# Performance work log

Measured on AMD Instinct MI355X. Metric: run time of the kernel, lower is better.

## Reference

```python
import jax, jax.numpy as jnp
import numpy as np

REG_M = 0.1     # reg_m_bregman
N_ITER = 30     # fixed MM iteration count (POT uses numItermax=1000 w/ early stop)
EPS = 1e-16     # POT's stabilizer added to the denominator


def setup_inputs() -> dict:
    key = jax.random.key(0)
    kx, ky = jax.random.split(key)
    x = jax.random.normal(kx, (4096, 256), dtype=jnp.float32)
    y = jax.random.normal(ky, (4096, 256), dtype=jnp.float32)
    # L2-normalize embeddings so squared distances lie in [0,4] and the
    # KL kernel exp(-M / (2*reg_m)) stays in a representable range.
    x = x / jnp.linalg.norm(x, axis=1, keepdims=True)
    y = y / jnp.linalg.norm(y, axis=1, keepdims=True)
    return {"x": x, "y": y}


def reference(x, y):
    m, n = x.shape[0], y.shape[0]
    # ot.dist default metric: squared euclidean  M[i,j] = ||x_i - y_j||^2
    M = (jnp.sum(x * x, axis=1)[:, None]
         + jnp.sum(y * y, axis=1)[None, :]
         - 2.0 * (x @ y.T))                                  # [m, n]
    a = jnp.full((m,), 1.0 / m, dtype=x.dtype)
    b = jnp.full((n,), 1.0 / n, dtype=x.dtype)
    # POT mm_unbalanced, div='kl', reg_m1=reg_m2=reg_m, reg=0:
    # r1 = r2 = 1/2, K = sqrt(a_i b_j) * exp(-M / (2*reg_m)), G0 = a (x) b,
    # G <- K * G / (sqrt(rowsum_i) * sqrt(colsum_j) + eps)
    K = jnp.sqrt(a[:, None] * b[None, :]) * jnp.exp(-M / (2.0 * REG_M))
    G0 = a[:, None] * b[None, :]

    def step(G, _):
        Gd = jnp.sqrt(G.sum(axis=1)[:, None] * G.sum(axis=0)[None, :]) + EPS
        return K * G / Gd, None

    Pi, _ = jax.lax.scan(step, G0, None, length=N_ITER)
    # (Pi @ M.T).mean() = sum_j (sum_i Pi[i,j]) * (sum_k M[k,j]) / m^2
    return jnp.dot(Pi.sum(axis=0), M.sum(axis=0)) / (m * m)
```

## Files before the change

### kernel.cpp

```cpp
#include <hip/hip_runtime.h>
#include <math.h>

#define MDIM 4096
#define NDIM 4096
#define DDIM 256
#define N_ITER 30

#define TWO_KAPPA 14.426950408889634
#define CLCONST  (-12.0 - TWO_KAPPA)

typedef __attribute__((ext_vector_type(8))) short bf16x8;
typedef __attribute__((ext_vector_type(4))) float f32x4;

__device__ __forceinline__ unsigned encf(float f) {
  unsigned u = __float_as_uint(f);
  return (u & 0x80000000u) ? ~u : (u | 0x80000000u);
}
__device__ __forceinline__ float decf(unsigned u) {
  return __uint_as_float((u & 0x80000000u) ? (u ^ 0x80000000u) : ~u);
}
__device__ __forceinline__ unsigned ldvu(const unsigned* p) { return *(const volatile unsigned*)p; }
__device__ __forceinline__ float    ldvf(const float* p)    { return *(const volatile float*)p; }

__global__ void norms_kernel(const float* __restrict__ x, const float* __restrict__ y,
                             float* __restrict__ xx, float* __restrict__ yy,
                             float* __restrict__ Sxx) {
  int wid = threadIdx.x >> 6, lane = threadIdx.x & 63;
  int row = blockIdx.x * 4 + wid;
  const float* src = (row < MDIM) ? x : y;
  int r = (row < MDIM) ? row : row - MDIM;
  const float4* p = (const float4*)(src + (size_t)r * DDIM);
  float4 v = p[lane];
  float s = v.x*v.x + v.y*v.y + v.z*v.z + v.w*v.w;
  #pragma unroll
  for (int off = 32; off; off >>= 1) s += __shfl_down(s, off);
  if (lane == 0) {
    if (row < MDIM) { xx[r] = s; atomicAdd(Sxx, s); }
    else            { yy[r] = s; }
  }
}

__global__ void sx_kernel(const float* __restrict__ x, float* __restrict__ sx) {
  int tx = threadIdx.x;
  int r0 = blockIdx.x * 16;
  float s = 0.f;
  #pragma unroll
  for (int r = 0; r < 16; ++r) s += x[(size_t)(r0 + r) * DDIM + tx];
  atomicAdd(&sx[tx], s);
}

__global__ void colM_kernel(const float* __restrict__ y, const float* __restrict__ sx,
                            const float* __restrict__ yy, const float* __restrict__ Sxx,
                            float* __restrict__ colM) {
  int wid = threadIdx.x >> 6, lane = threadIdx.x & 63;
  int j = blockIdx.x * 4 + wid;
  const float4* py = (const float4*)(y + (size_t)j * DDIM);
  const float4* ps = (const float4*)sx;
  float4 a = py[lane], b = ps[lane];
  float s = a.x*b.x + a.y*b.y + a.z*b.z + a.w*b.w;
  #pragma unroll
  for (int off = 32; off; off >>= 1) s += __shfl_down(s, off);
  if (lane == 0) colM[j] = *Sxx + (float)MDIM * yy[j] - 2.f * s;
}

__global__ void split_kernel(const float* __restrict__ x, const float* __restrict__ y,
                             ushort* __restrict__ xh, ushort* __restrict__ xl,
                             ushort* __restrict__ yh, ushort* __restrict__ yl) {
  int g = blockIdx.x * 256 + threadIdx.x;
  int e; const float4* src; ushort* dh; ushort* dl;
  if (g < 262144) { e = g;          src = (const float4*)x; dh = xh; dl = xl; }
  else            { e = g - 262144; src = (const float4*)y; dh = yh; dl = yl; }
  float4 v = src[e];
  float f[4] = {v.x, v.y, v.z, v.w};
  ushort hs[4], ls[4];
  #pragma unroll
  for (int i = 0; i < 4; ++i) {
    unsigned u = __float_as_uint(f[i]);
    unsigned hr = (u + 0x7FFFu + ((u >> 16) & 1u)) >> 16;
    hs[i] = (ushort)hr;
    float hf = __uint_as_float(hr << 16);
    float lo = f[i] - hf;
    unsigned ul = __float_as_uint(lo);
    unsigned lr = (ul + 0x7FFFu + ((ul >> 16) & 1u)) >> 16;
    ls[i] = (ushort)lr;
  }
  *(ushort4*)(dh + (size_t)e * 4) = make_ushort4(hs[0], hs[1], hs[2], hs[3]);
  *(ushort4*)(dl + (size_t)e * 4) = make_ushort4(ls[0], ls[1], ls[2], ls[3]);
}

#define GPAD 56
__global__ __launch_bounds__(256)
void gemm_mfma_kernel(const ushort* __restrict__ xh, const ushort* __restrict__ xl,
                      const ushort* __restrict__ yh, const ushort* __restrict__ yl,
                      short* __restrict__ D16, float* __restrict__ maxdot) {
  __shared__ ushort As[2][128][GPAD];
  __shared__ ushort Bs[2][128][GPAD];
  int tid = threadIdx.x;
  int lane = tid & 63, wid = tid >> 6;
  int bm = blockIdx.x & 31, bn = blockIdx.x >> 5;
  int wrow = (wid >> 1) * 64, wcol = (wid & 1) * 64;
  f32x4 acc[4][4] = {};

  int c0 = tid, c1 = tid + 256;
  int r0 = c0 >> 2, k80 = (c0 & 3) * 8;
  int r1 = c1 >> 2, k81 = (c1 & 3) * 8;
  const size_t arow0 = (size_t)(bm * 128 + r0) * DDIM;
  const size_t arow1 = (size_t)(bm * 128 + r1) * DDIM;
  const size_t brow0 = (size_t)(bn * 128 + r0) * DDIM;
  const size_t brow1 = (size_t)(bn * 128 + r1) * DDIM;

  for (int k0 = 0; k0 < DDIM; k0 += 32) {
    *(uint4*)&As[0][r0][k80] = *(const uint4*)(xh + arow0 + k0 + k80);
    *(uint4*)&As[0][r1][k81] = *(const uint4*)(xh + arow1 + k0 + k81);
    *(uint4*)&As[1][r0][k80] = *(const uint4*)(xl + arow0 + k0 + k80);
    *(uint4*)&As[1][r1][k81] = *(const uint4*)(xl + arow1 + k0 + k81);
    *(uint4*)&Bs[0][r0][k80] = *(const uint4*)(yh + brow0 + k0 + k80);
    *(uint4*)&Bs[0][r1][k81] = *(const uint4*)(yh + brow1 + k0 + k81);
    *(uint4*)&Bs[1][r0][k80] = *(const uint4*)(yl + brow0 + k0 + k80);
    *(uint4*)&Bs[1][r1][k81] = *(const uint4*)(yl + brow1 + k0 + k81);
    __syncthreads();
    int fr = lane & 15, kg = lane >> 4;
    bf16x8 ah[4], al[4], bh[4], bl[4];
    #pragma unroll
    for (int i = 0; i < 4; ++i) {
      ah[i] = *(const bf16x8*)&As[0][wrow + i * 16 + fr][kg * 8];
      al[i] = *(const bf16x8*)&As[1][wrow + i * 16 + fr][kg * 8];
      bh[i] = *(const bf16x8*)&Bs[0][wcol + i * 16 + fr][kg * 8];
      bl[i] = *(const bf16x8*)&Bs[1][wcol + i * 16 + fr][kg * 8];
    }
    #pragma unroll
    for (int i = 0; i < 4; ++i)
      #pragma unroll
      for (int j = 0; j < 4; ++j) {
        acc[i][j] = __builtin_amdgcn_mfma_f32_16x16x32_bf16(ah[i], bh[j], acc[i][j], 0, 0, 0);
        acc[i][j] = __builtin_amdgcn_mfma_f32_16x16x32_bf16(ah[i], bl[j], acc[i][j], 0, 0, 0);
        acc[i][j] = __builtin_amdgcn_mfma_f32_16x16x32_bf16(al[i], bh[j], acc[i][j], 0, 0, 0);
      }
    __syncthreads();
  }
  float tmax = -1.f;
  #pragma unroll
  for (int i = 0; i < 4; ++i) {
    #pragma unroll
    for (int j = 0; j < 4; ++j) {
      int col = bn * 128 + wcol + j * 16 + (lane & 15);
      #pragma unroll
      for (int r = 0; r < 4; ++r) {
        float d = acc[i][j][r];
        tmax = fmaxf(tmax, d);
        int q = __float2int_rn(fminf(fmaxf(d * 65536.f, -32767.f), 32767.f));
        int row = bm * 128 + wrow + i * 16 + (lane >> 4) * 4 + r;
        D16[(size_t)row * NDIM + col] = (short)q;
      }
    }
  }
  __shared__ float sm[4];
  #pragma unroll
  for (int off = 32; off; off >>= 1) tmax = fmaxf(tmax, __shfl_down(tmax, off));
  if (lane == 0) sm[wid] = tmax;
  __syncthreads();
  if (tid == 0) {
    float m = fmaxf(fmaxf(sm[0], sm[1]), fmaxf(sm[2], sm[3]));
    atomicMax((int*)maxdot, __float_as_int(fmaxf(m, 0.f)));
  }
}

__device__ __forceinline__ void gridbar(unsigned* cnt, unsigned* root, int b, int blk) {
  __syncthreads();
  if (threadIdx.x == 0) {
    unsigned* sc = cnt + ((b << 4) + (blk & 15)) * 16;
    unsigned old = __hip_atomic_fetch_add(sc, 1u, __ATOMIC_ACQ_REL, __HIP_MEMORY_SCOPE_AGENT);
    if (old == 15u) {
      __hip_atomic_fetch_add(root + b * 16, 1u, __ATOMIC_ACQ_REL, __HIP_MEMORY_SCOPE_AGENT);
    }
    while (__hip_atomic_load(root + b * 16, __ATOMIC_RELAXED, __HIP_MEMORY_SCOPE_AGENT) < 16u)
      __builtin_amdgcn_s_sleep(1);
    (void)__hip_atomic_load(root + b * 16, __ATOMIC_ACQUIRE, __HIP_MEMORY_SCOPE_AGENT);
  }
  __syncthreads();
}

__global__ __launch_bounds__(1024, 4)
void solve_kernel(const short* __restrict__ D16,
                  float* __restrict__ phi_g, float* __restrict__ psi_g,
                  const float* __restrict__ maxdot,
                  unsigned* psimaxS, unsigned* phimaxS,
                  const float* __restrict__ colM,
                  float* lossacc, float* __restrict__ out,
                  unsigned* cnt, unsigned* root) {
  __shared__ float vec_lds[4096];
  __shared__ float red[32][33];
  __shared__ float own[32];
  int tid = threadIdx.x;
  int blk = blockIdx.x;
  bool rowside = blk < 128;
  int lloc = tid & 31;
  int chunk = tid >> 5;
  int obase = (rowside ? blk : (blk - 128)) * 32;
  float md = maxdot[0];

  int2 d[32];
  if (rowside) {
    const short* src = D16 + (size_t)(obase + lloc) * NDIM + chunk * 128;
    #pragma unroll
    for (int g = 0; g < 32; ++g) d[g] = *(const int2*)(src + 4 * g);
  } else {
    int j = obase + lloc;
    #pragma unroll
    for (int g = 0; g < 32; ++g) {
      int rr = chunk * 128 + 4 * g;
      unsigned s0 = (unsigned short)(unsigned)D16[(size_t)(rr + 0) * NDIM + j];
      unsigned s1 = (unsigned short)(unsigned)D16[(size_t)(rr + 1) * NDIM + j];
      unsigned s2 = (unsigned short)(unsigned)D16[(size_t)(rr + 2) * NDIM + j];
      unsigned s3 = (unsigned short)(unsigned)D16[(size_t)(rr + 3) * NDIM + j];
      d[g].x = (int)(s0 | (s1 << 16));
      d[g].y = (int)(s2 | (s3 << 16));
    }
  }
  if (tid < 32) own[tid] = -6.f;

  for (int t = 1; t <= N_ITER; ++t) {
    float sD  = (float)((double)t * (TWO_KAPPA / 65536.0));
    float tCL = (float)((double)t * CLCONST);
    float s2k = (float)((double)t * TWO_KAPPA);
    float tLmax = fmaf(s2k, md, tCL);
    float psimax, phimax;
    if (t == 1) { psimax = phimax = -6.f; }
    else {
      unsigned up = 0, uf = 0;
      #pragma unroll
      for (int s = 0; s < 16; ++s) {
        unsigned a = ldvu(&psimaxS[(t << 4) + s]); up = a > up ? a : up;
        unsigned b = ldvu(&phimaxS[(t << 4) + s]); uf = b > uf ? b : uf;
      }
      psimax = decf(up); phimax = decf(uf);
    }
    float Sr = tLmax + psimax - 100.f;
    float Sc = tLmax + phimax - 100.f;
    float Wr = tCL - Sr;
    float Wc = tCL - Sc;
    float Sh = rowside ? Sr : Sc;

    {
      float add = rowside ? Wr : Wc;
      float4 v;
      if (t == 1) {
        float c = -6.f + add;
        v = make_float4(c, c, c, c);
      } else {
        const float* src = rowside ? psi_g : phi_g;
        v = *(const float4*)(src + tid * 4);
        v.x += add; v.y += add; v.z += add; v.w += add;
      }
      *(float4*)&vec_lds[tid * 4] = v;
    }
    __syncthreads();

    float acc = 0.f;
    #pragma unroll
    for (int g = 0; g < 32; ++g) {
      float4 pv = *(const float4*)&vec_lds[chunk * 128 + 4 * g];
      int2 dv = d[g];
      float d0 = (float)((short)(dv.x & 0xFFFF));
      float d1 = (float)(dv.x >> 16);
      float d2 = (float)((short)(dv.y & 0xFFFF));
      float d3 = (float)(dv.y >> 16);
      acc += exp2f(fmaf(d0, sD, pv.x));
      acc += exp2f(fmaf(d1, sD, pv.y));
      acc += exp2f(fmaf(d2, sD, pv.z));
      acc += exp2f(fmaf(d3, sD, pv.w));
    }
    red[lloc][chunk] = acc;
    __syncthreads();

    if (tid < 32) {
      float tot = 0.f;
      #pragma unroll
      for (int c = 0; c < 32; ++c) tot += red[tid][c];
      if (rowside || t < N_ITER) {
        float pn = 0.5f * (own[tid] - Sh - log2f(fmaxf(tot, 1e-30f)));
        own[tid] = pn;
        if (rowside) phi_g[obase + tid] = pn;
        else         psi_g[obase + tid] = pn;
        #pragma unroll
        for (int o = 16; o; o >>= 1) pn = fmaxf(pn, __shfl_down(pn, o));
        if (tid == 0) {
          unsigned* dst = rowside ? &phimaxS[((t + 1) << 4) + (blk & 15)]
                                  : &psimaxS[((t + 1) << 4) + (blk & 15)];
          atomicMax(dst, encf(pn));
        }
      } else {
        float contrib = exp2f(log2f(fmaxf(tot, 1e-30f)) + own[tid] + Sc
                              + log2f(colM[obase + tid]));
        #pragma unroll
        for (int o = 16; o; o >>= 1) contrib += __shfl_down(contrib, o);
        if (tid == 0) atomicAdd(&lossacc[blk & 15], contrib);
      }
    }
    gridbar(cnt, root, t - 1, blk);
  }
  if (blk == 0 && tid == 0) {
    float tot = 0.f;
    #pragma unroll
    for (int s = 0; s < 16; ++s) tot += ldvf(&lossacc[s]);
    out[0] = tot * (1.f / ((float)MDIM * (float)MDIM));
  }
}

extern "C" void kernel_launch(void* const* d_in, const int* in_sizes, int n_in,
                              void* d_out, int out_size, void* d_ws, size_t ws_size,
                              hipStream_t stream) {
  const float* x = (const float*)d_in[0];
  const float* y = (const float*)d_in[1];
  float* out = (float*)d_out;

  char* ws = (char*)d_ws;
  size_t off = 0;
  auto alloc = [&](size_t bytes) -> void* {
    void* p = ws + off;
    off += (bytes + 255) & ~(size_t)255;
    return p;
  };
  short*    D16     = (short*)alloc((size_t)MDIM * NDIM * 2);
  ushort*   xh      = (ushort*)alloc((size_t)MDIM * DDIM * 2);
  ushort*   xl      = (ushort*)alloc((size_t)MDIM * DDIM * 2);
  ushort*   yh      = (ushort*)alloc((size_t)NDIM * DDIM * 2);
  ushort*   yl      = (ushort*)alloc((size_t)NDIM * DDIM * 2);
  float*    xx      = (float*)alloc(MDIM * 4);
  float*    yy      = (float*)alloc(NDIM * 4);
  float*    sx      = (float*)alloc(DDIM * 4);
  float*    colM    = (float*)alloc(NDIM * 4);
  float*    Sxx     = (float*)alloc(4);
  float*    maxd    = (float*)alloc(4);
  unsigned* psimaxS = (unsigned*)alloc(64 * 16 * 4);
  unsigned* phimaxS = (unsigned*)alloc(64 * 16 * 4);
  float*    phi_g   = (float*)alloc(MDIM * 4);
  float*    psi_g   = (float*)alloc(NDIM * 4);
  float*    lossacc = (float*)alloc(16 * 4);
  unsigned* cnt     = (unsigned*)alloc(64 * 16 * 16 * 4);
  unsigned* root    = (unsigned*)alloc(64 * 16 * 4);

  hipMemsetAsync(Sxx, 0, 4, stream);
  hipMemsetAsync(maxd, 0, 4, stream);
  hipMemsetAsync(sx, 0, DDIM * 4, stream);
  hipMemsetAsync(psimaxS, 0, 64 * 16 * 4, stream);
  hipMemsetAsync(phimaxS, 0, 64 * 16 * 4, stream);
  hipMemsetAsync(lossacc, 0, 16 * 4, stream);
  hipMemsetAsync(cnt, 0, 64 * 16 * 16 * 4, stream);
  hipMemsetAsync(root, 0, 64 * 16 * 4, stream);

  norms_kernel<<<2048, 256, 0, stream>>>(x, y, xx, yy, Sxx);
  sx_kernel<<<256, 256, 0, stream>>>(x, sx);
  colM_kernel<<<1024, 256, 0, stream>>>(y, sx, yy, Sxx, colM);
  split_kernel<<<2048, 256, 0, stream>>>(x, y, xh, xl, yh, yl);
  gemm_mfma_kernel<<<1024, 256, 0, stream>>>(xh, xl, yh, yl, D16, maxd);

  void* kargs[] = {(void*)&D16, (void*)&phi_g, (void*)&psi_g,
                   (void*)&maxd, (void*)&psimaxS, (void*)&phimaxS,
                   (void*)&colM, (void*)&lossacc, (void*)&out,
                   (void*)&cnt, (void*)&root};
  hipLaunchCooperativeKernel((void*)solve_kernel, dim3(256), dim3(1024),
                             kargs, 0, stream);
}
```

Baseline: 1.006 ms.

## Replace grid barrier with per-side flag handshakes and double-buffered potentials

Removes the full grid barrier after every iteration. Row and column blocks now wait only on a counter flag from the opposite side, and the potentials are published into double-buffered arrays so producers can run one step ahead. The loss reduction is finalized by a counter-gated block instead of a post-barrier step, and the exp accumulation is split into four independent accumulators for more ILP. The code uses relaxed atomics plus s_waitcnt for ordering, which risks memory-visibility races; acquire semantics are not formally guaranteed.

```diff
diff --git a/kernel.cpp b/kernel.cpp
--- a/kernel.cpp
+++ b/kernel.cpp
@@ -19,8 +19,11 @@
 __device__ __forceinline__ float decf(unsigned u) {
   return __uint_as_float((u & 0x80000000u) ? (u ^ 0x80000000u) : ~u);
 }
-__device__ __forceinline__ unsigned ldvu(const unsigned* p) { return *(const volatile unsigned*)p; }
-__device__ __forceinline__ float    ldvf(const float* p)    { return *(const volatile float*)p; }
+
+#define AL_RLX(p)      __hip_atomic_load((p), __ATOMIC_RELAXED, __HIP_MEMORY_SCOPE_AGENT)
+#define AS_RLX(p, v)   __hip_atomic_store((p), (v), __ATOMIC_RELAXED, __HIP_MEMORY_SCOPE_AGENT)
+#define AADD_RLX(p, v) __hip_atomic_fetch_add((p), (v), __ATOMIC_RELAXED, __HIP_MEMORY_SCOPE_AGENT)
+#define AMAX_RLX(p, v) __hip_atomic_fetch_max((p), (v), __ATOMIC_RELAXED, __HIP_MEMORY_SCOPE_AGENT)
 
 __global__ void norms_kernel(const float* __restrict__ x, const float* __restrict__ y,
                              float* __restrict__ xx, float* __restrict__ yy,
@@ -165,32 +168,19 @@
   }
 }
 
-__device__ __forceinline__ void gridbar(unsigned* cnt, unsigned* root, int b, int blk) {
-  __syncthreads();
-  if (threadIdx.x == 0) {
-    unsigned* sc = cnt + ((b << 4) + (blk & 15)) * 16;
-    unsigned old = __hip_atomic_fetch_add(sc, 1u, __ATOMIC_ACQ_REL, __HIP_MEMORY_SCOPE_AGENT);
-    if (old == 15u) {
-      __hip_atomic_fetch_add(root + b * 16, 1u, __ATOMIC_ACQ_REL, __HIP_MEMORY_SCOPE_AGENT);
-    }
-    while (__hip_atomic_load(root + b * 16, __ATOMIC_RELAXED, __HIP_MEMORY_SCOPE_AGENT) < 16u)
-      __builtin_amdgcn_s_sleep(1);
-    (void)__hip_atomic_load(root + b * 16, __ATOMIC_ACQUIRE, __HIP_MEMORY_SCOPE_AGENT);
-  }
-  __syncthreads();
-}
-
 __global__ __launch_bounds__(1024, 4)
 void solve_kernel(const short* __restrict__ D16,
-                  float* __restrict__ phi_g, float* __restrict__ psi_g,
+                  float* __restrict__ phi_pub, float* __restrict__ psi_pub,
                   const float* __restrict__ maxdot,
-                  unsigned* psimaxS, unsigned* phimaxS,
+                  unsigned* rowMaxU, unsigned* colMaxU,
+                  unsigned* rowFlag, unsigned* colFlag,
                   const float* __restrict__ colM,
-                  float* lossacc, float* __restrict__ out,
-                  unsigned* cnt, unsigned* root) {
+                  float* lossacc, unsigned* lossdone,
+                  float* __restrict__ out) {
   __shared__ float vec_lds[4096];
   __shared__ float red[32][33];
   __shared__ float own[32];
+  __shared__ float sMax;
   int tid = threadIdx.x;
   int blk = blockIdx.x;
   bool rowside = blk < 128;
@@ -198,6 +188,13 @@
   int chunk = tid >> 5;
   int obase = (rowside ? blk : (blk - 128)) * 32;
   float md = maxdot[0];
+
+  unsigned* partnerFlag = rowside ? colFlag : rowFlag;
+  unsigned* partnerMaxU = rowside ? colMaxU : rowMaxU;
+  unsigned* myFlag      = rowside ? rowFlag : colFlag;
+  unsigned* myMaxU      = rowside ? rowMaxU : colMaxU;
+  const float* partnerPub = rowside ? psi_pub : phi_pub;
+  float*       myPub      = rowside ? phi_pub : psi_pub;
 
   int2 d[32];
   if (rowside) {
@@ -219,44 +216,46 @@
   }
   if (tid < 32) own[tid] = -6.f;
 
-  for (int t = 1; t <= N_ITER; ++t) {
+  int tEnd = rowside ? (N_ITER - 1) : N_ITER;
+  for (int t = 1; t <= tEnd; ++t) {
     float sD  = (float)((double)t * (TWO_KAPPA / 65536.0));
     float tCL = (float)((double)t * CLCONST);
     float s2k = (float)((double)t * TWO_KAPPA);
     float tLmax = fmaf(s2k, md, tCL);
-    float psimax, phimax;
-    if (t == 1) { psimax = phimax = -6.f; }
+
+    float partnerMax;
+    if (t == 1) partnerMax = -6.f;
     else {
-      unsigned up = 0, uf = 0;
-      #pragma unroll
-      for (int s = 0; s < 16; ++s) {
-        unsigned a = ldvu(&psimaxS[(t << 4) + s]); up = a > up ? a : up;
-        unsigned b = ldvu(&phimaxS[(t << 4) + s]); uf = b > uf ? b : uf;
-      }
-      psimax = decf(up); phimax = decf(uf);
-    }
-    float Sr = tLmax + psimax - 100.f;
-    float Sc = tLmax + phimax - 100.f;
-    float Wr = tCL - Sr;
-    float Wc = tCL - Sc;
-    float Sh = rowside ? Sr : Sc;
+      if (tid == 0) {
+        while (AL_RLX(partnerFlag + t * 16) < 128u)
+          __builtin_amdgcn_s_sleep(2);
+        sMax = decf(AL_RLX(partnerMaxU + t * 16));
+      }
+      __syncthreads();
+      partnerMax = sMax;
+    }
+    float Sh  = tLmax + partnerMax - 100.f;
+    float Wsh = tCL - Sh;
 
     {
-      float add = rowside ? Wr : Wc;
       float4 v;
       if (t == 1) {
-        float c = -6.f + add;
+        float c = -6.f + Wsh;
         v = make_float4(c, c, c, c);
       } else {
-        const float* src = rowside ? psi_g : phi_g;
-        v = *(const float4*)(src + tid * 4);
-        v.x += add; v.y += add; v.z += add; v.w += add;
+        const float* src = partnerPub + (size_t)(t & 1) * 4096 + tid * 4;
+        unsigned long long a = AL_RLX((const unsigned long long*)src);
+        unsigned long long b = AL_RLX((const unsigned long long*)(src + 2));
+        v.x = __uint_as_float((unsigned)a) + Wsh;
+        v.y = __uint_as_float((unsigned)(a >> 32)) + Wsh;
+        v.z = __uint_as_float((unsigned)b) + Wsh;
+        v.w = __uint_as_float((unsigned)(b >> 32)) + Wsh;
       }
       *(float4*)&vec_lds[tid * 4] = v;
     }
     __syncthreads();
 
-    float acc = 0.f;
+    float a0 = 0.f, a1 = 0.f, a2 = 0.f, a3 = 0.f;
     #pragma unroll
     for (int g = 0; g < 32; ++g) {
       float4 pv = *(const float4*)&vec_lds[chunk * 128 + 4 * g];
@@ -265,12 +264,12 @@
       float d1 = (float)(dv.x >> 16);
       float d2 = (float)((short)(dv.y & 0xFFFF));
       float d3 = (float)(dv.y >> 16);
-      acc += exp2f(fmaf(d0, sD, pv.x));
-      acc += exp2f(fmaf(d1, sD, pv.y));
-      acc += exp2f(fmaf(d2, sD, pv.z));
-      acc += exp2f(fmaf(d3, sD, pv.w));
-    }
-    red[lloc][chunk] = acc;
+      a0 += exp2f(fmaf(d0, sD, pv.x));
+      a1 += exp2f(fmaf(d1, sD, pv.y));
+      a2 += exp2f(fmaf(d2, sD, pv.z));
+      a3 += exp2f(fmaf(d3, sD, pv.w));
+    }
+    red[lloc][chunk] = (a0 + a1) + (a2 + a3);
     __syncthreads();
 
     if (tid < 32) {
@@ -280,30 +279,34 @@
       if (rowside || t < N_ITER) {
         float pn = 0.5f * (own[tid] - Sh - log2f(fmaxf(tot, 1e-30f)));
         own[tid] = pn;
-        if (rowside) phi_g[obase + tid] = pn;
-        else         psi_g[obase + tid] = pn;
+        AS_RLX(myPub + (size_t)((t + 1) & 1) * 4096 + obase + tid, pn);
+        float mx = pn;
         #pragma unroll
-        for (int o = 16; o; o >>= 1) pn = fmaxf(pn, __shfl_down(pn, o));
+        for (int o = 16; o; o >>= 1) mx = fmaxf(mx, __shfl_down(mx, o));
         if (tid == 0) {
-          unsigned* dst = rowside ? &phimaxS[((t + 1) << 4) + (blk & 15)]
-                                  : &psimaxS[((t + 1) << 4) + (blk & 15)];
-          atomicMax(dst, encf(pn));
+          AMAX_RLX(myMaxU + (t + 1) * 16, encf(mx));
+          asm volatile("s_waitcnt vmcnt(0)" ::: "memory");
+          AADD_RLX(myFlag + (t + 1) * 16, 1u);
         }
       } else {
-        float contrib = exp2f(log2f(fmaxf(tot, 1e-30f)) + own[tid] + Sc
+        float contrib = exp2f(log2f(fmaxf(tot, 1e-30f)) + own[tid] + Sh
                               + log2f(colM[obase + tid]));
         #pragma unroll
         for (int o = 16; o; o >>= 1) contrib += __shfl_down(contrib, o);
-        if (tid == 0) atomicAdd(&lossacc[blk & 15], contrib);
-      }
-    }
-    gridbar(cnt, root, t - 1, blk);
-  }
-  if (blk == 0 && tid == 0) {
-    float tot = 0.f;
-    #pragma unroll
-    for (int s = 0; s < 16; ++s) tot += ldvf(&lossacc[s]);
-    out[0] = tot * (1.f / ((float)MDIM * (float)MDIM));
+        if (tid == 0) {
+          AADD_RLX(&lossacc[blk & 15], contrib);
+          asm volatile("s_waitcnt vmcnt(0)" ::: "memory");
+          AADD_RLX(lossdone, 1u);
+          if (blk == 128) {
+            while (AL_RLX(lossdone) < 128u) __builtin_amdgcn_s_sleep(2);
+            float tot2 = 0.f;
+            #pragma unroll
+            for (int s = 0; s < 16; ++s) tot2 += AL_RLX(&lossacc[s]);
+            out[0] = tot2 * (1.f / ((float)MDIM * (float)MDIM));
+          }
+        }
+      }
+    }
   }
 }
 
@@ -332,22 +335,24 @@
   float*    colM    = (float*)alloc(NDIM * 4);
   float*    Sxx     = (float*)alloc(4);
   float*    maxd    = (float*)alloc(4);
-  unsigned* psimaxS = (unsigned*)alloc(64 * 16 * 4);
-  unsigned* phimaxS = (unsigned*)alloc(64 * 16 * 4);
-  float*    phi_g   = (float*)alloc(MDIM * 4);
-  float*    psi_g   = (float*)alloc(NDIM * 4);
+  float*    phi_pub = (float*)alloc(2 * MDIM * 4);
+  float*    psi_pub = (float*)alloc(2 * NDIM * 4);
+  unsigned* rowMaxU = (unsigned*)alloc(32 * 16 * 4);
+  unsigned* colMaxU = (unsigned*)alloc(32 * 16 * 4);
+  unsigned* rowFlag = (unsigned*)alloc(32 * 16 * 4);
+  unsigned* colFlag = (unsigned*)alloc(32 * 16 * 4);
   float*    lossacc = (float*)alloc(16 * 4);
-  unsigned* cnt     = (unsigned*)alloc(64 * 16 * 16 * 4);
-  unsigned* root    = (unsigned*)alloc(64 * 16 * 4);
+  unsigned* lossdone= (unsigned*)alloc(16 * 4);
 
   hipMemsetAsync(Sxx, 0, 4, stream);
   hipMemsetAsync(maxd, 0, 4, stream);
   hipMemsetAsync(sx, 0, DDIM * 4, stream);
-  hipMemsetAsync(psimaxS, 0, 64 * 16 * 4, stream);
-  hipMemsetAsync(phimaxS, 0, 64 * 16 * 4, stream);
+  hipMemsetAsync(rowMaxU, 0, 32 * 16 * 4, stream);
+  hipMemsetAsync(colMaxU, 0, 32 * 16 * 4, stream);
+  hipMemsetAsync(rowFlag, 0, 32 * 16 * 4, stream);
+  hipMemsetAsync(colFlag, 0, 32 * 16 * 4, stream);
   hipMemsetAsync(lossacc, 0, 16 * 4, stream);
-  hipMemsetAsync(cnt, 0, 64 * 16 * 16 * 4, stream);
-  hipMemsetAsync(root, 0, 64 * 16 * 4, stream);
+  hipMemsetAsync(lossdone, 0, 16 * 4, stream);
 
   norms_kernel<<<2048, 256, 0, stream>>>(x, y, xx, yy, Sxx);
   sx_kernel<<<256, 256, 0, stream>>>(x, sx);
@@ -355,10 +360,11 @@
   split_kernel<<<2048, 256, 0, stream>>>(x, y, xh, xl, yh, yl);
   gemm_mfma_kernel<<<1024, 256, 0, stream>>>(xh, xl, yh, yl, D16, maxd);
 
-  void* kargs[] = {(void*)&D16, (void*)&phi_g, (void*)&psi_g,
-                   (void*)&maxd, (void*)&psimaxS, (void*)&phimaxS,
-                   (void*)&colM, (void*)&lossacc, (void*)&out,
-                   (void*)&cnt, (void*)&root};
+  void* kargs[] = {(void*)&D16, (void*)&phi_pub, (void*)&psi_pub,
+                   (void*)&maxd, (void*)&rowMaxU, (void*)&colMaxU,
+                   (void*)&rowFlag, (void*)&colFlag,
+                   (void*)&colM, (void*)&lossacc, (void*)&lossdone,
+                   (void*)&out};
   hipLaunchCooperativeKernel((void*)solve_kernel, dim3(256), dim3(1024),
                              kargs, 0, stream);
 }
```

Result: slower. 1.027 ms (+2.1%).
